# Kernel tuning notes

Hardware: AMD Instinct MI355X
Metric: run time of the kernel (lower is better)

The kernel has to match this reference:

```python
import jax, jax.numpy as jnp
import numpy as np

B, N, C = 2, 20000, 256
TEST_MAX_BOX = 5000
IOU_THRESHOLDS = (0.4, 0.6, 0.8)
N_HIDDEN_LAYERS = 6  # six Conv1d(256,256,k=1)+LeakyReLU blocks in mask_w_layers


def setup_inputs() -> dict:
    key = jax.random.key(0)
    ks = jax.random.split(key, 8)
    # valid xyxy boxes: top-left in [0,900), w/h in [4,84)
    xy = jax.random.uniform(ks[0], (B, 2, N), dtype=jnp.float32) * 900.0
    wh = jax.random.uniform(ks[1], (B, 2, N), dtype=jnp.float32) * 80.0 + 4.0
    box = jnp.concatenate([xy, xy + wh], axis=1)              # [B,4,N]
    score = jax.random.uniform(ks[2], (B, 1, N), dtype=jnp.float32)
    feat = jax.random.normal(ks[3], (B, C, N), dtype=jnp.float32)
    W = jax.random.normal(ks[4], (N_HIDDEN_LAYERS, C, C), dtype=jnp.float32) * 0.02
    b = jnp.zeros((N_HIDDEN_LAYERS, C), dtype=jnp.float32)
    Wf = jax.random.normal(ks[5], (len(IOU_THRESHOLDS), C), dtype=jnp.float32) * 0.02
    bf = jnp.zeros((len(IOU_THRESHOLDS),), dtype=jnp.float32)
    return {"box": box, "score": score, "feat": feat, "W": W, "b": b, "Wf": Wf, "bf": bf}


def _box_iou(a, bxs):
    # a: [N,4], bxs: [M,4], xyxy -> [N,M] (torchvision ops.box_iou)
    area_a = (a[:, 2] - a[:, 0]) * (a[:, 3] - a[:, 1])
    area_b = (bxs[:, 2] - bxs[:, 0]) * (bxs[:, 3] - bxs[:, 1])
    lt = jnp.maximum(a[:, None, :2], bxs[None, :, :2])
    rb = jnp.minimum(a[:, None, 2:], bxs[None, :, 2:])
    wh = jnp.clip(rb - lt, 0.0)
    inter = wh[..., 0] * wh[..., 1]
    return inter / (area_a[:, None] + area_b[None, :] - inter)


def reference(box, score, feat, W, b, Wf, bf):
    # forward_test path of LMM
    boxT = jnp.swapaxes(box, 1, 2)                 # [B,N,4]
    s = jnp.swapaxes(score, 1, 2)[..., 0]          # [B,N]
    top_s, keep = jax.lax.top_k(s, TEST_MAX_BOX)   # [B,K] each, sorted desc
    boxK = jnp.take_along_axis(boxT, keep[..., None], axis=1)   # [B,K,4]
    featK = jnp.take_along_axis(feat, keep[:, None, :], axis=2)  # [B,C,K]

    iou = jax.vmap(_box_iou)(boxK, boxK)           # [B,K,K]
    idx = jnp.arange(TEST_MAX_BOX)
    masks = []
    for thr in IOU_THRESHOLDS:
        adjc = jnp.where(iou >= thr, 1.0, 0.0) * top_s[:, :, None]  # [B,K,K]
        max_idx = jnp.argmax(adjc, axis=1)                           # [B,K]
        masks.append((max_idx == idx[None, :]).astype(featK.dtype))
    masks = jnp.stack(masks, axis=1)               # [B,3,K]

    x = featK
    for l in range(N_HIDDEN_LAYERS):
        x = jax.nn.leaky_relu(jnp.einsum('oi,bik->bok', W[l], x) + b[l][:, None], 0.2)
    mask_w = jax.nn.softmax(jnp.einsum('oi,bik->bok', Wf, x) + bf[:, None], axis=1)  # [B,3,K]

    loc_max = jnp.sum(masks * mask_w, axis=1, keepdims=True)  # [B,1,K]
    return (loc_max, keep)
```

## Files before the change

kernel.cpp:

```cpp
#include <hip/hip_runtime.h>

#define B_  2
#define N_  20000
#define C_  256
#define K_  5000
#define M_  (B_ * K_)
#define CAP_ 5376
#define NBIN_ 2048
#define AST_ 264
#define RT_  21
#define RCH_ 7
#define RCT_ 3

typedef __attribute__((ext_vector_type(8))) short bf16x8;
typedef __attribute__((ext_vector_type(4))) float f32x4;
typedef __attribute__((ext_vector_type(2))) unsigned long long ull2;

__device__ __forceinline__ unsigned short f2bf(float x) {
  unsigned u = __float_as_uint(x);
  return (unsigned short)((u + 0x7fffu + ((u >> 16) & 1u)) >> 16);
}
__device__ __forceinline__ float bf2f(unsigned short h) {
  return __uint_as_float(((unsigned)h) << 16);
}
__device__ __forceinline__ unsigned fkey(float f) {
  unsigned u = __float_as_uint(f);
  return (u & 0x80000000u) ? ~u : (u | 0x80000000u);
}
__device__ __forceinline__ int binof(float s) {
  int b = (int)(s * 2048.0f);
  return b < 0 ? 0 : (b > 2047 ? 2047 : b);
}
__device__ __forceinline__ bf16x8 as_bf(uint4 v) {
  union { uint4 u; bf16x8 b; } c; c.u = v; return c.b;
}

__global__ __launch_bounds__(256) void k_prep(const float* __restrict__ W,
                                              unsigned short* __restrict__ Whi,
                                              int* __restrict__ nc,
                                              int* __restrict__ cnt2) {
  const int u = blockIdx.x;
  const int t = threadIdx.x;
  if (u >= 192) {
    if (u == 234) { if (t < B_) nc[t] = 0; return; }
    const int i = (u - 192) * 256 + t;
    if (i < B_ * CAP_) cnt2[i] = 0;
    return;
  }
  const int idx = u * 256 + t;
  const int lane = idx & 63;
  const int oi = (idx >> 6) & 1;
  const int ks = (idx >> 7) & 7;
  const int w = (idx >> 10) & 7;
  const int l = idx >> 13;
  const int o = w * 32 + oi * 16 + (lane & 15);
  const int k0 = ks * 32 + (lane >> 4) * 8;
  const float* src = W + ((size_t)(l * C_ + o)) * C_ + k0;
  float4 w0 = *(const float4*)&src[0];
  float4 w1 = *(const float4*)&src[4];
  const float wv[8] = {w0.x, w0.y, w0.z, w0.w, w1.x, w1.y, w1.z, w1.w};
  unsigned short hs[8];
#pragma unroll
  for (int q = 0; q < 8; ++q) hs[q] = f2bf(wv[q]);
  *(uint4*)&Whi[(size_t)idx * 8] = *(const uint4*)&hs[0];
}

__global__ __launch_bounds__(256) void k_selcomp(const float* __restrict__ score,
                                                 int* __restrict__ nc,
                                                 unsigned long long* __restrict__ ck,
                                                 int* __restrict__ rnk) {
  const int b = blockIdx.y;
  const float* s = score + b * N_;
  __shared__ int h[NBIN_];
  __shared__ int chs[256];
  __shared__ int res[1];
  const int t = threadIdx.x;
  for (int i = t; i < NBIN_; i += 256) h[i] = 0;
  __syncthreads();
  for (int i = t; i < N_; i += 256) atomicAdd(&h[binof(s[i])], 1);
  __syncthreads();
  int sum = 0;
#pragma unroll
  for (int j = 0; j < 8; ++j) sum += h[t * 8 + j];
  chs[t] = sum;
  __syncthreads();
  for (int off = 1; off < 256; off <<= 1) {
    int v = chs[t] + ((t + off < 256) ? chs[t + off] : 0);
    __syncthreads();
    chs[t] = v;
    __syncthreads();
  }
  const int above = (t + 1 < 256) ? chs[t + 1] : 0;
  if (above < K_ && K_ <= chs[t]) {
    int acc = above;
    for (int i = 7; i >= 0; --i) {
      const int bin = t * 8 + i;
      if (acc + h[bin] >= K_) { res[0] = bin; break; }
      acc += h[bin];
    }
  }
  __syncthreads();
  const int selB = res[0];
  const int n = blockIdx.x * 256 + t;
  if (n < N_) {
    rnk[b * N_ + n] = K_;
    const float sv = s[n];
    if (binof(sv) >= selB) {
      const int pos = atomicAdd(&nc[b], 1);
      if (pos < CAP_)
        ck[b * CAP_ + pos] =
            ((unsigned long long)fkey(sv) << 32) | (unsigned)(N_ - 1 - n);
    }
  }
}

__global__ __launch_bounds__(256) void k_rank2(const int* __restrict__ nc,
                                               const unsigned long long* __restrict__ ck,
                                               int* __restrict__ cnt2) {
  const int b = blockIdx.z;
  int S = nc[b]; if (S > CAP_) S = CAP_;
  __shared__ unsigned long long sk[256];
  const int t = threadIdx.x;
  const int j = blockIdx.x * 256 + t;
  const unsigned long long* kb = ck + b * CAP_;
  const unsigned long long myk = (j < S) ? kb[j] : 0ULL;
  int c = 0;
  const int nt = (S + 255) >> 8;
  int t0 = blockIdx.y * RCT_, t1 = t0 + RCT_;
  if (t1 > nt) t1 = nt;
  for (int tt = t0; tt < t1; ++tt) {
    const int gi = tt * 256 + t;
    unsigned long long kk = (gi < S) ? kb[gi] : 0ULL;
    __syncthreads();
    sk[t] = kk;
    __syncthreads();
#pragma unroll 8
    for (int ii = 0; ii < 256; ii += 2) {
      ull2 v = *(const ull2*)&sk[ii];
      c += (int)(v.x > myk) + (int)(v.y > myk);
    }
  }
  if (j < S && c > 0) atomicAdd(&cnt2[b * CAP_ + j], c);
}

__global__ __launch_bounds__(256) void k_scatter2(const int* __restrict__ nc,
                                                  const unsigned long long* __restrict__ ck,
                                                  const int* __restrict__ cnt2,
                                                  const float* __restrict__ box,
                                                  int* __restrict__ keep_i,
                                                  float* __restrict__ out_keep,
                                                  int* __restrict__ rnk,
                                                  float* __restrict__ boxK,
                                                  unsigned* __restrict__ maxiou) {
  const int b = blockIdx.y;
  int S = nc[b]; if (S > CAP_) S = CAP_;
  const int j = blockIdx.x * 256 + threadIdx.x;
  if (j >= S) return;
  const int c = cnt2[b * CAP_ + j];
  if (c >= K_) return;
  const int n = N_ - 1 - (int)(ck[b * CAP_ + j] & 0xffffffffu);
  keep_i[b * K_ + c] = n;
  out_keep[b * K_ + c] = (float)n;
  rnk[b * N_ + n] = c;
  const float* bb = box + (size_t)b * 4 * N_;
  float4 v;
  v.x = bb[n]; v.y = bb[N_ + n]; v.z = bb[2 * N_ + n]; v.w = bb[3 * N_ + n];
  ((float4*)boxK)[b * K_ + c] = v;
  maxiou[b * K_ + c] = 0u;
}

__global__ __launch_bounds__(256) void k_ioug(const float* __restrict__ boxK,
                                              unsigned* __restrict__ maxiou,
                                              const int* __restrict__ rnk,
                                              const float* __restrict__ feat,
                                              unsigned short* __restrict__ Xhi) {
  __shared__ __align__(16) char arena[16640];
  const int u = blockIdx.x;
  const int t = threadIdx.x;
  if (u < 420) {
    const int b = u / 210;
    const int p = u % 210;
    int jt = 0;
    while ((jt + 1) * (jt + 2) / 2 <= p) ++jt;
    const int it = p - jt * (jt + 1) / 2;
    float* sx0 = (float*)arena;
    float* sy0 = sx0 + 256; float* sx1 = sy0 + 256;
    float* sy1 = sx1 + 256; float* sa = sy1 + 256;
    const int gi0 = it * 256;
    const int gl = gi0 + t;
    if (gl < K_) {
      float4 v = ((const float4*)boxK)[b * K_ + gl];
      sx0[t] = v.x; sy0[t] = v.y; sx1[t] = v.z; sy1[t] = v.w;
      sa[t] = __fmul_rn(__fsub_rn(v.z, v.x), __fsub_rn(v.w, v.y));
    } else {
      sx0[t] = 1e30f; sy0[t] = 1e30f; sx1[t] = -1e30f; sy1[t] = -1e30f;
      sa[t] = 0.f;
    }
    __syncthreads();
    const int j = jt * 256 + t;
    if (j >= K_) return;
    float4 v = ((const float4*)boxK)[b * K_ + j];
    const float aj = __fmul_rn(__fsub_rn(v.z, v.x), __fsub_rn(v.w, v.y));
    float mx = 0.f;
    int lim = j - gi0;
    if (lim > 256) lim = 256;
    for (int ii = 0; ii < lim; ++ii) {
      float ltx = fmaxf(sx0[ii], v.x);
      float lty = fmaxf(sy0[ii], v.y);
      float rbx = fminf(sx1[ii], v.z);
      float rby = fminf(sy1[ii], v.w);
      float wx = fmaxf(__fsub_rn(rbx, ltx), 0.f);
      float wy = fmaxf(__fsub_rn(rby, lty), 0.f);
      float inter = __fmul_rn(wx, wy);
      if (inter > 0.f) {
        float uni = __fsub_rn(__fadd_rn(sa[ii], aj), inter);
        mx = fmaxf(mx, __fdiv_rn(inter, uni));
      }
    }
    if (mx > 0.f) atomicMax(&maxiou[b * K_ + j], __float_as_uint(mx));
  } else {
    const int v2 = u - 420;
    const int b = v2 / 1252;
    const int rem = v2 % 1252;
    const int c0 = (rem / 313) * 64;
    const int n0 = (rem % 313) * 64;
    float* T = (float*)arena;
    const int nl = t & 63, wq = t >> 6;
#pragma unroll
    for (int r = 0; r < 16; ++r) {
      const int cl = r * 4 + wq;
      const int n = n0 + nl;
      T[nl * 65 + cl] =
          (n < N_) ? feat[((size_t)(b * C_ + c0 + cl)) * N_ + n] : 0.f;
    }
    __syncthreads();
    const int nn = n0 + (t >> 2);
    if (nn >= N_) return;
    const int r = rnk[b * N_ + nn];
    if (r >= K_) return;
    const int cseg = (t & 3) * 16;
    unsigned short hb[16];
#pragma unroll
    for (int i = 0; i < 16; ++i)
      hb[i] = f2bf(T[(t >> 2) * 65 + cseg + i]);
    const size_t base = (size_t)(b * K_ + r) * C_ + c0 + cseg;
    *(uint4*)&Xhi[base] = *(const uint4*)&hb[0];
    *(uint4*)&Xhi[base + 8] = *(const uint4*)&hb[8];
  }
}

__global__ __launch_bounds__(512, 2) void k_mlp6(
    const unsigned short* __restrict__ Whi,
    const float* __restrict__ bias, const float* __restrict__ Wf,
    const float* __restrict__ bf, const unsigned* __restrict__ maxiou,
    const unsigned short* __restrict__ Xhi,
    float* __restrict__ out_loc) {
  __shared__ unsigned short act_hi[32 * AST_];
  __shared__ float swf[768];
  const int t = threadIdx.x;
  const int m0 = blockIdx.x * 32;

  {
    const int r = t >> 4;
    const int cs = (t & 15) * 16;
    const size_t g = (size_t)(m0 + r) * C_ + cs;
    *(uint4*)&act_hi[r * AST_ + cs] = *(const uint4*)&Xhi[g];
    *(uint4*)&act_hi[r * AST_ + cs + 8] = *(const uint4*)&Xhi[g + 8];
  }
  for (int i = t; i < 768; i += 512) swf[i] = Wf[i];
  __syncthreads();

  const int lane = t & 63;
  const int w = t >> 6;
  const int quad = lane >> 4, l15 = lane & 15;

  for (int l = 0; l < 6; ++l) {
    const size_t wbase = (size_t)(l * 8 + w) * 8192 + (size_t)lane * 8;
    f32x4 acc[2][2];
#pragma unroll
    for (int mi = 0; mi < 2; ++mi)
#pragma unroll
      for (int oi = 0; oi < 2; ++oi) acc[mi][oi] = (f32x4)0.f;
    uint4 nwh[2];
#pragma unroll
    for (int oi = 0; oi < 2; ++oi)
      nwh[oi] = *(const uint4*)&Whi[wbase + oi * 512];
#pragma unroll
    for (int ks = 0; ks < 8; ++ks) {
      bf16x8 wh[2];
#pragma unroll
      for (int oi = 0; oi < 2; ++oi) wh[oi] = as_bf(nwh[oi]);
      if (ks < 7) {
        const size_t nb = wbase + (size_t)(ks + 1) * 1024;
#pragma unroll
        for (int oi = 0; oi < 2; ++oi)
          nwh[oi] = *(const uint4*)&Whi[nb + oi * 512];
      }
      bf16x8 Ah[2];
#pragma unroll
      for (int mi = 0; mi < 2; ++mi)
        Ah[mi] = *(const bf16x8*)&act_hi[(mi * 16 + l15) * AST_ + ks * 32 + quad * 8];
#pragma unroll
      for (int mi = 0; mi < 2; ++mi)
#pragma unroll
        for (int oi = 0; oi < 2; ++oi)
          acc[mi][oi] = __builtin_amdgcn_mfma_f32_16x16x32_bf16(Ah[mi], wh[oi], acc[mi][oi], 0, 0, 0);
    }
    __syncthreads();
#pragma unroll
    for (int oi = 0; oi < 2; ++oi) {
      const int col = w * 32 + oi * 16 + l15;
      const float bb = bias[l * C_ + col];
#pragma unroll
      for (int mi = 0; mi < 2; ++mi)
#pragma unroll
        for (int r = 0; r < 4; ++r) {
          float y = acc[mi][oi][r] + bb;
          y = fmaxf(y, 0.2f * y);
          act_hi[(mi * 16 + quad * 4 + r) * AST_ + col] = f2bf(y);
        }
    }
    __syncthreads();
  }

  const int r = t >> 4;
  const int part = t & 15;
  const int m = m0 + r;
  float a0 = 0.f, a1 = 0.f, a2 = 0.f;
  for (int c = part * 16; c < part * 16 + 16; c += 2) {
    const unsigned hv = *(const unsigned*)&act_hi[r * AST_ + c];
    const float x0 = __uint_as_float((hv & 0xffffu) << 16);
    const float x1 = __uint_as_float(hv & 0xffff0000u);
    a0 += swf[c] * x0 + swf[c + 1] * x1;
    a1 += swf[256 + c] * x0 + swf[256 + c + 1] * x1;
    a2 += swf[512 + c] * x0 + swf[512 + c + 1] * x1;
  }
#pragma unroll
  for (int off = 1; off < 16; off <<= 1) {
    a0 += __shfl_xor(a0, off);
    a1 += __shfl_xor(a1, off);
    a2 += __shfl_xor(a2, off);
  }
  if (part == 0 && m < M_) {
    a0 += bf[0]; a1 += bf[1]; a2 += bf[2];
    const float mxv = fmaxf(a0, fmaxf(a1, a2));
    const float e0 = expf(a0 - mxv);
    const float e1 = expf(a1 - mxv);
    const float e2 = expf(a2 - mxv);
    const float inv = 1.f / (e0 + e1 + e2);
    const float miou = __uint_as_float(maxiou[m]);
    float loc = 0.f;
    if (miou < 0.4f) loc += e0;
    if (miou < 0.6f) loc += e1;
    if (miou < 0.8f) loc += e2;
    out_loc[m] = loc * inv;
  }
}

extern "C" void kernel_launch(void* const* d_in, const int* in_sizes, int n_in,
                              void* d_out, int out_size, void* d_ws, size_t ws_size,
                              hipStream_t stream) {
  const float* box   = (const float*)d_in[0];
  const float* score = (const float*)d_in[1];
  const float* feat  = (const float*)d_in[2];
  const float* W     = (const float*)d_in[3];
  const float* bias  = (const float*)d_in[4];
  const float* Wf    = (const float*)d_in[5];
  const float* bf    = (const float*)d_in[6];

  float* out = (float*)d_out;
  float* out_loc  = out;
  float* out_keep = out + M_;

  char* ws = (char*)d_ws;
  int*            keep_i = (int*)(ws + 0);
  float*          boxK   = (float*)(ws + 40960);
  unsigned*       maxiou = (unsigned*)(ws + 201216);
  unsigned short* Whi    = (unsigned short*)(ws + 241664);
  unsigned short* XtA_hi = (unsigned short*)(ws + 1814528);
  int*                rnk    = (int*)(ws + 12169216);
  unsigned long long* ck     = (unsigned long long*)(ws + 12329216);
  int*                cnt2   = (int*)(ws + 12415232);
  int*                nc     = (int*)(ws + 12458240);

  k_prep<<<235, 256, 0, stream>>>(W, Whi, nc, cnt2);
  k_selcomp<<<dim3(79, B_), 256, 0, stream>>>(score, nc, ck, rnk);
  k_rank2<<<dim3(RT_, RCH_, B_), 256, 0, stream>>>(nc, ck, cnt2);
  k_scatter2<<<dim3(RT_, B_), 256, 0, stream>>>(nc, ck, cnt2, box, keep_i,
                                                out_keep, rnk, boxK, maxiou);
  k_ioug<<<2924, 256, 0, stream>>>(boxK, maxiou, rnk, feat, XtA_hi);
  k_mlp6<<<313, 512, 0, stream>>>(Whi, bias, Wf, bf, maxiou, XtA_hi, out_loc);
}
```

Before: 190.4 us.

## Fuse top-k selection into two kernels with per-chunk ballot compaction

Replaces the atomic-counter compaction with a deterministic per-256-chunk ballot/popcount compaction, and folds the weight bf16 packing into the same launch. Rank counting and scatter now happen in one kernel: each block ranks its chunk's candidates against all chunks' candidates, which removes the cnt2 zeroing, the global atomics, and two kernel launches. In exchange, every rank block loops over all 79 chunks, reading unused slots, and does its rank work in a single block per chunk rather than splitting it across blocks.

```diff
diff --git a/kernel.cpp b/kernel.cpp
--- a/kernel.cpp
+++ b/kernel.cpp
@@ -5,12 +5,9 @@
 #define C_  256
 #define K_  5000
 #define M_  (B_ * K_)
-#define CAP_ 5376
 #define NBIN_ 2048
 #define AST_ 264
-#define RT_  21
-#define RCH_ 7
-#define RCT_ 3
+#define NCH_ 79
 
 typedef __attribute__((ext_vector_type(8))) short bf16x8;
 typedef __attribute__((ext_vector_type(4))) float f32x4;
@@ -35,138 +32,130 @@
   union { uint4 u; bf16x8 b; } c; c.u = v; return c.b;
 }
 
-__global__ __launch_bounds__(256) void k_prep(const float* __restrict__ W,
-                                              unsigned short* __restrict__ Whi,
-                                              int* __restrict__ nc,
-                                              int* __restrict__ cnt2) {
+__global__ __launch_bounds__(256) void k_selpack(const float* __restrict__ score,
+                                                 const float* __restrict__ W,
+                                                 unsigned short* __restrict__ Whi,
+                                                 unsigned long long* __restrict__ ck,
+                                                 int* __restrict__ sc,
+                                                 int* __restrict__ rnk) {
   const int u = blockIdx.x;
   const int t = threadIdx.x;
-  if (u >= 192) {
-    if (u == 234) { if (t < B_) nc[t] = 0; return; }
-    const int i = (u - 192) * 256 + t;
-    if (i < B_ * CAP_) cnt2[i] = 0;
-    return;
-  }
-  const int idx = u * 256 + t;
-  const int lane = idx & 63;
-  const int oi = (idx >> 6) & 1;
-  const int ks = (idx >> 7) & 7;
-  const int w = (idx >> 10) & 7;
-  const int l = idx >> 13;
-  const int o = w * 32 + oi * 16 + (lane & 15);
-  const int k0 = ks * 32 + (lane >> 4) * 8;
-  const float* src = W + ((size_t)(l * C_ + o)) * C_ + k0;
-  float4 w0 = *(const float4*)&src[0];
-  float4 w1 = *(const float4*)&src[4];
-  const float wv[8] = {w0.x, w0.y, w0.z, w0.w, w1.x, w1.y, w1.z, w1.w};
-  unsigned short hs[8];
-#pragma unroll
-  for (int q = 0; q < 8; ++q) hs[q] = f2bf(wv[q]);
-  *(uint4*)&Whi[(size_t)idx * 8] = *(const uint4*)&hs[0];
-}
-
-__global__ __launch_bounds__(256) void k_selcomp(const float* __restrict__ score,
-                                                 int* __restrict__ nc,
-                                                 unsigned long long* __restrict__ ck,
-                                                 int* __restrict__ rnk) {
+  if (u < NCH_ * B_) {
+    const int b = u / NCH_, ch = u % NCH_;
+    const float* s = score + b * N_;
+    __shared__ int h[NBIN_];
+    __shared__ int chs[256];
+    __shared__ int res[1];
+    __shared__ int wtot[4], woff[4];
+    for (int i = t; i < NBIN_; i += 256) h[i] = 0;
+    __syncthreads();
+    for (int i = t; i < N_; i += 256) atomicAdd(&h[binof(s[i])], 1);
+    __syncthreads();
+    int sum = 0;
+#pragma unroll
+    for (int j = 0; j < 8; ++j) sum += h[t * 8 + j];
+    chs[t] = sum;
+    __syncthreads();
+    for (int off = 1; off < 256; off <<= 1) {
+      int v = chs[t] + ((t + off < 256) ? chs[t + off] : 0);
+      __syncthreads();
+      chs[t] = v;
+      __syncthreads();
+    }
+    const int above = (t + 1 < 256) ? chs[t + 1] : 0;
+    if (above < K_ && K_ <= chs[t]) {
+      int acc = above;
+      for (int i = 7; i >= 0; --i) {
+        const int bin = t * 8 + i;
+        if (acc + h[bin] >= K_) { res[0] = bin; break; }
+        acc += h[bin];
+      }
+    }
+    __syncthreads();
+    const int selB = res[0];
+    const int n = ch * 256 + t;
+    bool pred = false;
+    unsigned long long key = 0ULL;
+    if (n < N_) {
+      rnk[b * N_ + n] = K_;
+      const float sv = s[n];
+      pred = (binof(sv) >= selB);
+      key = ((unsigned long long)fkey(sv) << 32) | (unsigned)(N_ - 1 - n);
+    }
+    const unsigned long long mask = __ballot(pred);
+    const int lane = t & 63, wv = t >> 6;
+    if (lane == 0) wtot[wv] = __popcll(mask);
+    __syncthreads();
+    if (t == 0) {
+      int a = 0;
+#pragma unroll
+      for (int i = 0; i < 4; ++i) { woff[i] = a; a += wtot[i]; }
+      sc[b * NCH_ + ch] = a;
+    }
+    __syncthreads();
+    if (pred) {
+      const int pos = woff[wv] + __popcll(mask & ((1ULL << lane) - 1ULL));
+      ck[(size_t)(b * NCH_ + ch) * 256 + pos] = key;
+    }
+  } else {
+    const int idx = (u - NCH_ * B_) * 256 + t;
+    const int lane = idx & 63;
+    const int oi = (idx >> 6) & 1;
+    const int ks = (idx >> 7) & 7;
+    const int w = (idx >> 10) & 7;
+    const int l = idx >> 13;
+    const int o = w * 32 + oi * 16 + (lane & 15);
+    const int k0 = ks * 32 + (lane >> 4) * 8;
+    const float* src = W + ((size_t)(l * C_ + o)) * C_ + k0;
+    float4 w0 = *(const float4*)&src[0];
+    float4 w1 = *(const float4*)&src[4];
+    const float wv4[8] = {w0.x, w0.y, w0.z, w0.w, w1.x, w1.y, w1.z, w1.w};
+    unsigned short hs[8];
+#pragma unroll
+    for (int q = 0; q < 8; ++q) hs[q] = f2bf(wv4[q]);
+    *(uint4*)&Whi[(size_t)idx * 8] = *(const uint4*)&hs[0];
+  }
+}
+
+__global__ __launch_bounds__(256) void k_rankscat(
+    const unsigned long long* __restrict__ ck, const int* __restrict__ sc,
+    const float* __restrict__ box, int* __restrict__ keep_i,
+    float* __restrict__ out_keep, int* __restrict__ rnk,
+    float* __restrict__ boxK, unsigned* __restrict__ maxiou) {
   const int b = blockIdx.y;
-  const float* s = score + b * N_;
-  __shared__ int h[NBIN_];
-  __shared__ int chs[256];
-  __shared__ int res[1];
+  const int jch = blockIdx.x;
   const int t = threadIdx.x;
-  for (int i = t; i < NBIN_; i += 256) h[i] = 0;
+  __shared__ unsigned long long sk[256];
+  __shared__ int scl[NCH_];
+  for (int i = t; i < NCH_; i += 256) scl[i] = sc[b * NCH_ + i];
   __syncthreads();
-  for (int i = t; i < N_; i += 256) atomicAdd(&h[binof(s[i])], 1);
-  __syncthreads();
-  int sum = 0;
-#pragma unroll
-  for (int j = 0; j < 8; ++j) sum += h[t * 8 + j];
-  chs[t] = sum;
-  __syncthreads();
-  for (int off = 1; off < 256; off <<= 1) {
-    int v = chs[t] + ((t + off < 256) ? chs[t + off] : 0);
-    __syncthreads();
-    chs[t] = v;
-    __syncthreads();
-  }
-  const int above = (t + 1 < 256) ? chs[t + 1] : 0;
-  if (above < K_ && K_ <= chs[t]) {
-    int acc = above;
-    for (int i = 7; i >= 0; --i) {
-      const int bin = t * 8 + i;
-      if (acc + h[bin] >= K_) { res[0] = bin; break; }
-      acc += h[bin];
-    }
-  }
-  __syncthreads();
-  const int selB = res[0];
-  const int n = blockIdx.x * 256 + t;
-  if (n < N_) {
-    rnk[b * N_ + n] = K_;
-    const float sv = s[n];
-    if (binof(sv) >= selB) {
-      const int pos = atomicAdd(&nc[b], 1);
-      if (pos < CAP_)
-        ck[b * CAP_ + pos] =
-            ((unsigned long long)fkey(sv) << 32) | (unsigned)(N_ - 1 - n);
-    }
-  }
-}
-
-__global__ __launch_bounds__(256) void k_rank2(const int* __restrict__ nc,
-                                               const unsigned long long* __restrict__ ck,
-                                               int* __restrict__ cnt2) {
-  const int b = blockIdx.z;
-  int S = nc[b]; if (S > CAP_) S = CAP_;
-  __shared__ unsigned long long sk[256];
-  const int t = threadIdx.x;
-  const int j = blockIdx.x * 256 + t;
-  const unsigned long long* kb = ck + b * CAP_;
-  const unsigned long long myk = (j < S) ? kb[j] : 0ULL;
+  const bool valid = t < scl[jch];
+  const unsigned long long myk =
+      valid ? ck[(size_t)(b * NCH_ + jch) * 256 + t] : 0ULL;
   int c = 0;
-  const int nt = (S + 255) >> 8;
-  int t0 = blockIdx.y * RCT_, t1 = t0 + RCT_;
-  if (t1 > nt) t1 = nt;
-  for (int tt = t0; tt < t1; ++tt) {
-    const int gi = tt * 256 + t;
-    unsigned long long kk = (gi < S) ? kb[gi] : 0ULL;
-    __syncthreads();
-    sk[t] = kk;
-    __syncthreads();
-#pragma unroll 8
-    for (int ii = 0; ii < 256; ii += 2) {
+  for (int ic = 0; ic < NCH_; ++ic) {
+    const int sci = scl[ic];
+    __syncthreads();
+    sk[t] = ck[(size_t)(b * NCH_ + ic) * 256 + t];
+    __syncthreads();
+    int ii = 0;
+    for (; ii + 1 < sci; ii += 2) {
       ull2 v = *(const ull2*)&sk[ii];
       c += (int)(v.x > myk) + (int)(v.y > myk);
     }
-  }
-  if (j < S && c > 0) atomicAdd(&cnt2[b * CAP_ + j], c);
-}
-
-__global__ __launch_bounds__(256) void k_scatter2(const int* __restrict__ nc,
-                                                  const unsigned long long* __restrict__ ck,
-                                                  const int* __restrict__ cnt2,
-                                                  const float* __restrict__ box,
-                                                  int* __restrict__ keep_i,
-                                                  float* __restrict__ out_keep,
-                                                  int* __restrict__ rnk,
-                                                  float* __restrict__ boxK,
-                                                  unsigned* __restrict__ maxiou) {
-  const int b = blockIdx.y;
-  int S = nc[b]; if (S > CAP_) S = CAP_;
-  const int j = blockIdx.x * 256 + threadIdx.x;
-  if (j >= S) return;
-  const int c = cnt2[b * CAP_ + j];
-  if (c >= K_) return;
-  const int n = N_ - 1 - (int)(ck[b * CAP_ + j] & 0xffffffffu);
-  keep_i[b * K_ + c] = n;
-  out_keep[b * K_ + c] = (float)n;
-  rnk[b * N_ + n] = c;
-  const float* bb = box + (size_t)b * 4 * N_;
-  float4 v;
-  v.x = bb[n]; v.y = bb[N_ + n]; v.z = bb[2 * N_ + n]; v.w = bb[3 * N_ + n];
-  ((float4*)boxK)[b * K_ + c] = v;
-  maxiou[b * K_ + c] = 0u;
+    if (ii < sci) c += (int)(sk[ii] > myk);
+  }
+  if (valid && c < K_) {
+    const int n = N_ - 1 - (int)(myk & 0xffffffffu);
+    keep_i[b * K_ + c] = n;
+    out_keep[b * K_ + c] = (float)n;
+    rnk[b * N_ + n] = c;
+    const float* bb = box + (size_t)b * 4 * N_;
+    float4 v;
+    v.x = bb[n]; v.y = bb[N_ + n]; v.z = bb[2 * N_ + n]; v.w = bb[3 * N_ + n];
+    ((float4*)boxK)[b * K_ + c] = v;
+    maxiou[b * K_ + c] = 0u;
+  }
 }
 
 __global__ __launch_bounds__(256) void k_ioug(const float* __restrict__ boxK,
@@ -378,16 +367,13 @@
   unsigned*       maxiou = (unsigned*)(ws + 201216);
   unsigned short* Whi    = (unsigned short*)(ws + 241664);
   unsigned short* XtA_hi = (unsigned short*)(ws + 1814528);
-  int*                rnk    = (int*)(ws + 12169216);
-  unsigned long long* ck     = (unsigned long long*)(ws + 12329216);
-  int*                cnt2   = (int*)(ws + 12415232);
-  int*                nc     = (int*)(ws + 12458240);
-
-  k_prep<<<235, 256, 0, stream>>>(W, Whi, nc, cnt2);
-  k_selcomp<<<dim3(79, B_), 256, 0, stream>>>(score, nc, ck, rnk);
-  k_rank2<<<dim3(RT_, RCH_, B_), 256, 0, stream>>>(nc, ck, cnt2);
-  k_scatter2<<<dim3(RT_, B_), 256, 0, stream>>>(nc, ck, cnt2, box, keep_i,
-                                                out_keep, rnk, boxK, maxiou);
+  int*                rnk = (int*)(ws + 12169216);
+  unsigned long long* ck  = (unsigned long long*)(ws + 12330240);
+  int*                sc  = (int*)(ws + 12654080);
+
+  k_selpack<<<NCH_ * B_ + 192, 256, 0, stream>>>(score, W, Whi, ck, sc, rnk);
+  k_rankscat<<<dim3(NCH_, B_), 256, 0, stream>>>(ck, sc, box, keep_i, out_keep,
+                                                 rnk, boxK, maxiou);
   k_ioug<<<2924, 256, 0, stream>>>(boxK, maxiou, rnk, feat, XtA_hi);
   k_mlp6<<<313, 512, 0, stream>>>(Whi, bias, Wf, bf, maxiou, XtA_hi, out_loc);
 }
```

After: 265.4 us. 1.39x slower.
